# Optimization experiments

Measured on AMD Instinct MI355X. Metric: run time of the kernel, lower is better.

The kernel has to match this reference:

```python
import jax, jax.numpy as jnp
import numpy as np

N, E = 100000, 1600000
IN_CH, HID, HEADS, OUT_CH = 128, 32, 2, 40
NEG_SLOPE = 0.2
BN_EPS = 1e-5


def _param(key, shape, scale=0.1):
    return scale * jax.random.normal(key, shape, dtype=jnp.float32)


def setup_inputs() -> dict:
    key = jax.random.key(0)
    ks = jax.random.split(key, 24)
    x = jax.random.normal(ks[0], (N, IN_CH), dtype=jnp.float32)
    edge_index = jax.random.randint(ks[1], (2, E), 0, N, dtype=jnp.int32)
    d0 = HEADS * HID  # 64
    inp = {
        'x': x, 'edge_index': edge_index,
        # conv0: in 128 -> 32 per head, concat -> 64
        'W0': _param(ks[2], (IN_CH, HEADS * HID)),
        'as0': _param(ks[3], (HEADS, HID)), 'ad0': _param(ks[4], (HEADS, HID)),
        'b0': jnp.zeros((d0,), jnp.float32),
        'g0': jnp.ones((d0,), jnp.float32), 'bt0': jnp.zeros((d0,), jnp.float32),
        # conv1: 64 -> 32 per head, concat -> 64
        'W1': _param(ks[5], (d0, HEADS * HID)),
        'as1': _param(ks[6], (HEADS, HID)), 'ad1': _param(ks[7], (HEADS, HID)),
        'b1': jnp.zeros((d0,), jnp.float32),
        'g1': jnp.ones((d0,), jnp.float32), 'bt1': jnp.zeros((d0,), jnp.float32),
        # conv2: 64 -> 40 per head, mean over heads -> 40
        'W2': _param(ks[8], (d0, HEADS * OUT_CH)),
        'as2': _param(ks[9], (HEADS, OUT_CH)), 'ad2': _param(ks[10], (HEADS, OUT_CH)),
        'b2': jnp.zeros((OUT_CH,), jnp.float32),
    }
    return inp


def gat_conv(x, src, dst, W, a_src, a_dst, bias, out_ch, concat):
    n = x.shape[0]
    h = (x @ W).reshape(n, HEADS, out_ch)            # [N,H,C]
    alpha_src = jnp.sum(h * a_src, axis=-1)          # [N,H]
    alpha_dst = jnp.sum(h * a_dst, axis=-1)          # [N,H]
    e = jax.nn.leaky_relu(alpha_src[src] + alpha_dst[dst], NEG_SLOPE)  # [E,H]
    # softmax over incoming edges per destination node (self loops guarantee >=1 edge)
    m = jax.ops.segment_max(e, dst, num_segments=n)
    e = jnp.exp(e - m[dst])
    s = jax.ops.segment_sum(e, dst, num_segments=n)
    alpha = e / s[dst]                                # [E,H]
    msg = h[src] * alpha[:, :, None]                  # [E,H,C]
    out = jax.ops.segment_sum(msg, dst, num_segments=n)  # [N,H,C]
    out = out.reshape(n, HEADS * out_ch) if concat else out.mean(axis=1)
    return out + bias


def batch_norm(x, gamma, beta):
    mu = jnp.mean(x, axis=0)
    var = jnp.mean(jnp.square(x - mu), axis=0)
    return gamma * (x - mu) * jax.lax.rsqrt(var + BN_EPS) + beta


def reference(x, edge_index, W0, as0, ad0, b0, g0, bt0,
              W1, as1, ad1, b1, g1, bt1, W2, as2, ad2, b2):
    n = x.shape[0]
    loops = jnp.arange(n, dtype=edge_index.dtype)
    src = jnp.concatenate([edge_index[0], loops])
    dst = jnp.concatenate([edge_index[1], loops])
    h = gat_conv(x, src, dst, W0, as0, ad0, b0, HID, True)
    h = jax.nn.elu(batch_norm(h, g0, bt0))
    h = gat_conv(h, src, dst, W1, as1, ad1, b1, HID, True)
    h = jax.nn.elu(batch_norm(h, g1, bt1))
    return gat_conv(h, src, dst, W2, as2, ad2, b2, OUT_CH, False)
```

## Files before the change

### kernel.cpp

```cpp
#include <hip/hip_runtime.h>
#include <hip/hip_bf16.h>
#include <math.h>


#define NNODES 100000
#define NEDGES 1600000
#define ENTOT  (NEDGES + NNODES)
#define NEG_SLOPE 0.2f
#define BN_EPS 1e-5f

#define NRANGE 8
#define RSIZE  (NNODES/NRANGE)
#define BCAP   262144
#define PBLK   2048
#define NB2    32
#define BSL    8192

typedef unsigned short u16;
typedef unsigned int u32;
typedef unsigned long long u64;
typedef __attribute__((ext_vector_type(8))) short short8;
typedef __attribute__((ext_vector_type(4))) float f32x4;

__device__ __forceinline__ float b2f(u16 u){ union{u32 i; float f;} v; v.i=((u32)u)<<16; return v.f; }
__device__ __forceinline__ float blo(u32 u){ union{u32 i; float f;} v; v.i=u<<16; return v.f; }
__device__ __forceinline__ float bhi(u32 u){ union{u32 i; float f;} v; v.i=u&0xffff0000u; return v.f; }
__device__ __forceinline__ u16 f2b(float x){ __hip_bfloat16 b=__float2bfloat16(x); return *(u16*)&b; }
__device__ __forceinline__ float ldf(const void* p, int i, int f){
  return f ? ((const float*)p)[i] : b2f(((const u16*)p)[i]);
}

__global__ void k_detect(const u16* __restrict__ x, int* __restrict__ flag){
  __shared__ int bad;
  if(threadIdx.x==0) bad=0;
  __syncthreads();
  int cnt=0;
  for(int i=threadIdx.x;i<4096;i+=256){
    u16 v = x[2*i];
    int ex = (v>>7)&0xff;
    if(ex==0xff || (ex==0 && (v&0x7fff)!=0)) cnt++;
  }
  atomicAdd(&bad,cnt);
  __syncthreads();
  if(threadIdx.x==0) flag[0] = (bad>4)?1:0;
}

__global__ __launch_bounds__(256) void k_part2(
    const int* __restrict__ ei, int* __restrict__ gptr, u32* __restrict__ bkt){
  __shared__ int lcnt[NRANGE], gbase[NRANGE];
  int t=threadIdx.x;
  if(t<NRANGE) lcnt[t]=0;
  __syncthreads();
  const int CH=(ENTOT+PBLK-1)/PBLK;
  int beg=blockIdx.x*CH, end=beg+CH; if(end>ENTOT) end=ENTOT;
  int nd[4], ns[4], nr[4], ne=0;
  for(int i=beg+t; i<end; i+=256){
    int d=(i<NEDGES)? ei[NEDGES+i] : (i-NEDGES);
    int s=(i<NEDGES)? ei[i] : d;
    nd[ne]=d; ns[ne]=s; ne++;
  }
  #pragma unroll 4
  for(int k=0;k<ne;k++) nr[k]=atomicAdd(&lcnt[nd[k]/RSIZE],1);
  __syncthreads();
  if(t<NRANGE) gbase[t]=atomicAdd(&gptr[t],lcnt[t]);
  __syncthreads();
  #pragma unroll 4
  for(int k=0;k<ne;k++){
    int r=nd[k]/RSIZE;
    u32 e = ((u32)(nd[k]-r*RSIZE)<<17) | (u32)ns[k];
    __builtin_nontemporal_store(e, &bkt[(size_t)r*BCAP + gbase[r] + nr[k]]);
  }
}

__global__ __launch_bounds__(256) void k_hist4(
    const u32* __restrict__ bkt, const int* __restrict__ gptr, int* __restrict__ lhist){
  __shared__ int lh[RSIZE];
  int t=threadIdx.x;
  for(int i=t;i<RSIZE;i+=256) lh[i]=0;
  __syncthreads();
  int r = blockIdx.x & (NRANGE-1);
  int c = blockIdx.x >> 3;
  int n = gptr[r];
  int per=(n+NB2-1)/NB2;
  int beg=c*per, end=beg+per; if(end>n) end=n;
  const u32* bp = bkt + (size_t)r*BCAP;
  for(int i=beg+t;i<end;i+=256) atomicAdd(&lh[bp[i]>>17],1);
  __syncthreads();
  int* out = lhist + (size_t)(r*NB2+c)*RSIZE;
  for(int i=t;i<RSIZE;i+=256) out[i]=lh[i];
}

__global__ __launch_bounds__(256) void k_sumscan(int* __restrict__ lhist, int* __restrict__ cnt){
  int n = blockIdx.x*256 + threadIdx.x;
  if(n>=NNODES) return;
  int r = n/RSIZE, i = n - r*RSIZE;
  int* base = lhist + (size_t)r*NB2*RSIZE + i;
  int run=0;
  #pragma unroll 8
  for(int c=0;c<NB2;c++){
    int v = base[(size_t)c*RSIZE];
    base[(size_t)c*RSIZE] = run;
    run += v;
  }
  cnt[n]=run;
}

#define SCAN_M (NNODES+1)
#define SCAN_NB ((SCAN_M + 2047)/2048)

__global__ void k_scan_a(const int* __restrict__ cnt, int* __restrict__ bsum){
  __shared__ int red[256];
  int b=blockIdx.x, t=threadIdx.x;
  int base = b*2048 + t*8;
  int s=0;
  #pragma unroll
  for(int j=0;j<8;j++){ int idx=base+j; s += (idx<NNODES)? cnt[idx]:0; }
  red[t]=s; __syncthreads();
  for(int o=128;o>0;o>>=1){ if(t<o) red[t]+=red[t+o]; __syncthreads(); }
  if(t==0) bsum[b]=red[0];
}

__global__ void k_scan_b(int* bsum){
  if(threadIdx.x==0){
    int run=0;
    for(int i=0;i<SCAN_NB;i++){ int v=bsum[i]; bsum[i]=run; run+=v; }
  }
}

__global__ void k_scan_c(const int* __restrict__ cnt, const int* __restrict__ bsum,
                         int* __restrict__ row_ptr){
  __shared__ int lds[256];
  int b=blockIdx.x, t=threadIdx.x;
  int base=b*2048+t*8;
  int v[8]; int s=0;
  #pragma unroll
  for(int j=0;j<8;j++){ int idx=base+j; int x=(idx<NNODES)?cnt[idx]:0; v[j]=s; s+=x; }
  lds[t]=s; __syncthreads();
  for(int o=1;o<256;o<<=1){
    int other=0; if(t>=o) other=lds[t-o];
    __syncthreads();
    lds[t]+=other;
    __syncthreads();
  }
  int texcl = lds[t] - s;
  int off0 = bsum[b] + texcl;
  #pragma unroll
  for(int j=0;j<8;j++){ int idx=base+j; if(idx<SCAN_M) row_ptr[idx]=off0+v[j]; }
}

__global__ __launch_bounds__(256) void k_scatter4(
    const u32* __restrict__ bkt, const int* __restrict__ gptr,
    const int* __restrict__ row_ptr, const int* __restrict__ lhist,
    int* __restrict__ col){
  __shared__ int lofs[RSIZE];
  int t=threadIdx.x;
  int r = blockIdx.x & (NRANGE-1);
  int c = blockIdx.x >> 3;
  int lo = r*RSIZE;
  const int* cb = lhist + (size_t)(r*NB2+c)*RSIZE;
  for(int i=t;i<RSIZE;i+=256) lofs[i] = row_ptr[lo+i] + cb[i];
  __syncthreads();
  int n = gptr[r];
  int per=(n+NB2-1)/NB2;
  int beg=c*per, end=beg+per; if(end>n) end=n;
  const u32* bp = bkt + (size_t)r*BCAP;
  for(int i=beg+t;i<end;i+=256){
    u32 e=bp[i];
    int pos=atomicAdd(&lofs[e>>17],1);
    col[pos]=(int)(e & 0x1FFFF);
  }
}

__global__ __launch_bounds__(256) void k_binsort(
    const int* __restrict__ row_ptr, const int* __restrict__ col,
    int* __restrict__ col2){
  __shared__ int lcol[BSL];
  int t = threadIdx.x;
  int blk0 = blockIdx.x*256;
  int d1 = blk0+256; if(d1>NNODES) d1=NNODES;
  int s0 = row_ptr[blk0], s1 = row_ptr[d1];
  int n = s1 - s0;
  bool fit = (n<=BSL);
  if(fit){ for(int i=t;i<n;i+=256) lcol[i]=col[s0+i]; }
  __syncthreads();
  int d = blk0 + t;
  if(d<NNODES){
    int b0=row_ptr[d], b1=row_ptr[d+1];
    u64 cntp=0;
    for(int j=b0;j<b1;j++){
      int c = fit ? lcol[j-s0] : col[j];
      cntp += 1ull << ((c/RSIZE)*8);
    }
    u64 offp=0; u32 run=0;
    #pragma unroll
    for(int sb=0;sb<8;sb++){
      offp |= (u64)(run&0xffu) << (sb*8);
      run += (u32)((cntp >> (sb*8)) & 0xff);
    }
    for(int j=b0;j<b1;j++){
      int c = fit ? lcol[j-s0] : col[j];
      int sb = c/RSIZE;
      int pos = b0 + (int)((offp>>(sb*8))&0xff);
      offp += 1ull << (sb*8);
      col2[pos]=c;
    }
  }
}

template<int K, int OUTC, int HID, bool XEXT, bool BN>
__global__ __launch_bounds__(256) void k_gemm_mfma(
    const void* __restrict__ xin, const void* __restrict__ W,
    const void* __restrict__ avs, const void* __restrict__ avd,
    const float2* __restrict__ bnab,
    u16* __restrict__ hout, float* __restrict__ asrc, float* __restrict__ adst,
    const int* __restrict__ flagp)
{
  const int f = flagp[0];
  constexpr int KP = K+8;
  constexpr int RS = OUTC+8;
  constexpr int NT = OUTC/16;
  constexpr int KQ = K/32;
  __shared__ __align__(16) u16 WT[OUTC*KP];
  __shared__ __align__(16) u16 HROW[4*16*RS];
  __shared__ float AVb[2*OUTC];
  __shared__ float2 BB[K];
  int t=threadIdx.x;
  const u16* Wu=(const u16*)W; const float* Wf=(const float*)W;
  for(int i8=t*8; i8<K*OUTC; i8+=256*8){
    int k=i8/OUTC, c0=i8-k*OUTC;
    u16 w8[8];
    if(f){
      const float* wp=Wf+i8;
      float4 a=*(const float4*)wp, b=*(const float4*)(wp+4);
      w8[0]=f2b(a.x);w8[1]=f2b(a.y);w8[2]=f2b(a.z);w8[3]=f2b(a.w);
      w8[4]=f2b(b.x);w8[5]=f2b(b.y);w8[6]=f2b(b.z);w8[7]=f2b(b.w);
    } else {
      uint4 q=*(const uint4*)(Wu+i8);
      w8[0]=q.x&0xffff;w8[1]=q.x>>16;w8[2]=q.y&0xffff;w8[3]=q.y>>16;
      w8[4]=q.z&0xffff;w8[5]=q.z>>16;w8[6]=q.w&0xffff;w8[7]=q.w>>16;
    }
    #pragma unroll
    for(int u=0;u<8;u++) WT[(c0+u)*KP + k] = w8[u];
  }
  for(int idx=t; idx<2*OUTC; idx+=256)
    AVb[idx] = (idx<OUTC)? ldf(avs,idx,f) : ldf(avd,idx-OUTC,f);
  if(BN) for(int idx=t; idx<K; idx+=256) BB[idx]=bnab[idx];
  __syncthreads();

  int wv=t>>6, lane=t&63;
  int m=lane&15, quad=lane>>4;
  int grow0 = blockIdx.x*64 + wv*16;
  int growA = grow0 + m;
  bool avalid = growA < NNODES;
  int growC = avalid ? growA : 0;

  f32x4 acc[NT] = {};
  #pragma unroll
  for(int kq=0;kq<KQ;kq++){
    int k0 = kq*32 + quad*8;
    union{ u32 u[4]; short8 s8; } A;
    if(XEXT && f==1){
      const float* xr=(const float*)xin + (size_t)growC*K + k0;
      float4 p=*(const float4*)xr, q=*(const float4*)(xr+4);
      A.u[0]=f2b(p.x)|((u32)f2b(p.y)<<16);
      A.u[1]=f2b(p.z)|((u32)f2b(p.w)<<16);
      A.u[2]=f2b(q.x)|((u32)f2b(q.y)<<16);
      A.u[3]=f2b(q.z)|((u32)f2b(q.w)<<16);
    } else {
      uint4 q=*(const uint4*)((const u16*)xin + (size_t)growC*K + k0);
      A.u[0]=q.x; A.u[1]=q.y; A.u[2]=q.z; A.u[3]=q.w;
    }
    if(BN){
      #pragma unroll
      for(int j=0;j<4;j++){
        float lo=b2f(A.u[j]&0xffff), hi=b2f(A.u[j]>>16);
        float2 c1=BB[k0+2*j], c2=BB[k0+2*j+1];
        lo=c1.x*lo+c1.y; lo = lo>0.f? lo : __expf(lo)-1.f;
        hi=c2.x*hi+c2.y; hi = hi>0.f? hi : __expf(hi)-1.f;
        A.u[j]=f2b(lo)|((u32)f2b(hi)<<16);
      }
    }
    #pragma unroll
    for(int nt=0;nt<NT;nt++){
      union{ uint4 q; short8 s8; } Bf;
      Bf.q = *(const uint4*)&WT[(nt*16+m)*KP + k0];
      acc[nt] = __builtin_amdgcn_mfma_f32_16x16x32_bf16(A.s8, Bf.s8, acc[nt], 0,0,0);
    }
  }
  u16* hr = &HROW[wv*16*RS];
  #pragma unroll
  for(int nt=0;nt<NT;nt++){
    #pragma unroll
    for(int reg=0;reg<4;reg++)
      hr[(quad*4+reg)*RS + nt*16+m] = f2b(acc[nt][reg]);
  }
  __syncthreads();
  {
    int row=lane&15, task=quad, head=task&1, sd=task>>1;
    float p=0.f;
    const u16* hrow=&hr[row*RS + head*HID];
    const float* av=&AVb[sd*OUTC + head*HID];
    #pragma unroll 8
    for(int c=0;c<HID;c++) p += b2f(hrow[c])*av[c];
    int grow=grow0+row;
    if(grow<NNODES){ (sd? adst:asrc)[grow*2+head]=p; }
  }
  {
    constexpr int CH8 = OUTC/8;
    for(int idx=lane; idx<16*CH8; idx+=64){
      int rr=idx/CH8, c8=idx-rr*CH8;
      int grow=grow0+rr;
      if(grow<NNODES)
        *(uint4*)(hout + (size_t)grow*OUTC + c8*8) = *(const uint4*)&hr[rr*RS + c8*8];
    }
  }
}

template<int OUTC, bool FINAL>
__global__ __launch_bounds__(256) void k_aggf(
  const int* __restrict__ row_ptr, const int* __restrict__ col2,
  const u16* __restrict__ hin, const float* __restrict__ asrcf,
  const float2* __restrict__ adst2, const void* __restrict__ bias,
  u16* __restrict__ houtb, void* __restrict__ outv, const int* __restrict__ flagp)
{
  const int f = flagp[0];
  __shared__ float vbuf[FINAL?32:1][84];
  int t = threadIdx.x;
  int g  = t>>3;
  int cg = t&7;
  int rr = blockIdx.x & 7, jb = blockIdx.x >> 3;
  int lim = RSIZE - jb*32;
  bool ok = g < lim;
  int d = rr*RSIZE + jb*32 + g;
  int base=0, deg=0;
  float2 adv = make_float2(0.f,0.f);
  if(ok){
    base = row_ptr[d];
    deg  = row_ptr[d+1] - base;
    adv  = adst2[d];
  }
  const int* cp  = col2 + base;
  const u16* hcg = hin + cg*8;
  float acc[8]={0,0,0,0,0,0,0,0};

  if(!FINAL){
    int ho = (cg>=4)?1:0;
    float aown = ho ? adv.y : adv.x;
    float s=0.f;
    for(int ph=0; ph<4; ++ph){
      int beg = (deg*ph)>>2;
      int end = (deg*(ph+1))>>2;
      for(int j=beg; j<end; j+=2){
        int c0 = cp[j];
        bool v1 = (j+1)<end;
        int c1 = cp[v1 ? j+1 : j];
        float sa = asrcf[c0*2+ho];
        float sb = asrcf[c1*2+ho];
        uint4 h0 = *(const uint4*)(hcg + (size_t)c0*OUTC);
        uint4 h1 = *(const uint4*)(hcg + (size_t)c1*OUTC);
        float e0 = sa+aown; e0 = fmaxf(e0, NEG_SLOPE*e0); e0 = fminf(e0,60.f);
        float e1 = sb+aown; e1 = fmaxf(e1, NEG_SLOPE*e1); e1 = fminf(e1,60.f);
        float p0 = __expf(e0), p1 = __expf(e1);
        if(!v1) p1 = 0.f;
        s += p0 + p1;
        acc[0] += p0*blo(h0.x) + p1*blo(h1.x);
        acc[1] += p0*bhi(h0.x) + p1*bhi(h1.x);
        acc[2] += p0*blo(h0.y) + p1*blo(h1.y);
        acc[3] += p0*bhi(h0.y) + p1*bhi(h1.y);
        acc[4] += p0*blo(h0.z) + p1*blo(h1.z);
        acc[5] += p0*bhi(h0.z) + p1*bhi(h1.z);
        acc[6] += p0*blo(h0.w) + p1*blo(h1.w);
        acc[7] += p0*bhi(h0.w) + p1*bhi(h1.w);
      }
      __syncthreads();
    }
    float inv = s>0.f ? 1.f/s : 0.f;
    if(ok){
      u16 o8[8];
      #pragma unroll
      for(int k=0;k<8;k++) o8[k]=f2b(acc[k]*inv + ldf(bias,cg*8+k,f));
      uint4 ov;
      ov.x=(u32)o8[0]|((u32)o8[1]<<16); ov.y=(u32)o8[2]|((u32)o8[3]<<16);
      ov.z=(u32)o8[4]|((u32)o8[5]<<16); ov.w=(u32)o8[6]|((u32)o8[7]<<16);
      *(uint4*)(houtb + (size_t)d*64 + cg*8) = ov;
    }
  } else {
    const float2* asrc2 = (const float2*)asrcf;
    const u16* hxg = hin + 64 + cg*2;
    float accx0=0.f, accx1=0.f;
    float s0=0.f, s1=0.f;
    for(int ph=0; ph<4; ++ph){
      int beg = (deg*ph)>>2;
      int end = (deg*(ph+1))>>2;
      for(int j=beg; j<end; j+=2){
        int c0 = cp[j];
        bool v1 = (j+1)<end;
        int c1 = cp[v1 ? j+1 : j];
        float2 sa = asrc2[c0];
        float2 sv = asrc2[c1];
        const u16* hp0 = hcg + (size_t)c0*OUTC;
        const u16* hp1 = hcg + (size_t)c1*OUTC;
        uint4 h0 = *(const uint4*)hp0;
        uint4 h1 = *(const uint4*)hp1;
        float e0 = sa.x+adv.x; e0 = fmaxf(e0, NEG_SLOPE*e0); e0 = fminf(e0,60.f);
        float e1 = sa.y+adv.y; e1 = fmaxf(e1, NEG_SLOPE*e1); e1 = fminf(e1,60.f);
        float p0 = __expf(e0), p1 = __expf(e1);
        float q0 = sv.x+adv.x; q0 = fmaxf(q0, NEG_SLOPE*q0); q0 = fminf(q0,60.f);
        float q1 = sv.y+adv.y; q1 = fmaxf(q1, NEG_SLOPE*q1); q1 = fminf(q1,60.f);
        float r0 = __expf(q0), r1 = __expf(q1);
        if(!v1){ r0=0.f; r1=0.f; }
        s0 += p0 + r0; s1 += p1 + r1;
        float pa = (cg<5)? p0 : p1;
        float pb = (cg<5)? r0 : r1;
        acc[0] += pa*blo(h0.x) + pb*blo(h1.x);
        acc[1] += pa*bhi(h0.x) + pb*bhi(h1.x);
        acc[2] += pa*blo(h0.y) + pb*blo(h1.y);
        acc[3] += pa*bhi(h0.y) + pb*bhi(h1.y);
        acc[4] += pa*blo(h0.z) + pb*blo(h1.z);
        acc[5] += pa*bhi(h0.z) + pb*bhi(h1.z);
        acc[6] += pa*blo(h0.w) + pb*blo(h1.w);
        acc[7] += pa*bhi(h0.w) + pb*bhi(h1.w);
        ushort2 ha = *(const ushort2*)(hxg + (size_t)c0*OUTC);
        ushort2 hb = *(const ushort2*)(hxg + (size_t)c1*OUTC);
        accx0 += p1*b2f(ha.x) + r1*b2f(hb.x);
        accx1 += p1*b2f(ha.y) + r1*b2f(hb.y);
      }
      __syncthreads();
    }
    float inv0 = s0>0.f?1.f/s0:0.f, inv1 = s1>0.f?1.f/s1:0.f;
    if(ok){
      #pragma unroll
      for(int k=0;k<8;k++)
        vbuf[g][cg*8+k] = acc[k]*((cg<5)?inv0:inv1);
      vbuf[g][64+cg*2]   = accx0*inv1;
      vbuf[g][64+cg*2+1] = accx1*inv1;
    }
    __syncthreads();
    for(int idx=t; idx<32*40; idx+=256){
      int gg=idx/40, ch=idx-gg*40;
      if(gg<lim){
        int dd = rr*RSIZE + jb*32 + gg;
        float res = 0.5f*(vbuf[gg][ch] + vbuf[gg][40+ch]) + ldf(bias,ch,f);
        if(f) ((float*)outv)[(size_t)dd*40+ch] = res;
        else  ((__hip_bfloat16*)outv)[(size_t)dd*40+ch] = __float2bfloat16(res);
      }
    }
  }
}

__global__ __launch_bounds__(256) void k_bnstats(const u16* __restrict__ h, float* __restrict__ stats){
  __shared__ float red[4][128];
  int t=threadIdx.x; int c=t&63; int g=t>>6;
  float s=0.f,q=0.f;
  for(int r=blockIdx.x*4+g; r<NNODES; r+=gridDim.x*4){
    float v=b2f(h[(size_t)r*64+c]); s+=v; q+=v*v;
  }
  red[g][c]=s; red[g][64+c]=q;
  __syncthreads();
  if(t<128){
    float tot=red[0][t]+red[1][t]+red[2][t]+red[3][t];
    atomicAdd(&stats[t], tot);
  }
}

__global__ void k_bnfinal(const float* __restrict__ stats,
                          const void* __restrict__ gm, const void* __restrict__ bt,
                          float2* __restrict__ bnab, const int* __restrict__ flagp){
  const int f = flagp[0];
  int c=threadIdx.x;
  if(c>=64) return;
  float mu=stats[c]*(1.0f/NNODES);
  float var=stats[64+c]*(1.0f/NNODES)-mu*mu;
  var = var>0.f?var:0.f;
  float A = ldf(gm,c,f)*rsqrtf(var+BN_EPS);
  float B = ldf(bt,c,f) - A*mu;
  bnab[c]=make_float2(A,B);
}

extern "C" void kernel_launch(void* const* d_in, const int* in_sizes, int n_in,
                              void* d_out, int out_size, void* d_ws, size_t ws_size,
                              hipStream_t stream){
  const void* x  =d_in[0];
  const int* ei =(const int*)d_in[1];
  const void* W0 =d_in[2];  const void* as0=d_in[3];  const void* ad0=d_in[4];
  const void* b0 =d_in[5];  const void* g0 =d_in[6];  const void* bt0=d_in[7];
  const void* W1 =d_in[8];  const void* as1=d_in[9];  const void* ad1=d_in[10];
  const void* b1 =d_in[11]; const void* g1 =d_in[12]; const void* bt1=d_in[13];
  const void* W2 =d_in[14]; const void* as2=d_in[15]; const void* ad2=d_in[16];
  const void* b2 =d_in[17];

  char* ws=(char*)d_ws;
  size_t off=0;
  auto alloc=[&](size_t bytes)->void*{ void* p=ws+off; off+=(bytes+255)&~(size_t)255; return p; };
  int*    flag   =(int*)   alloc(256);
  int*    row_ptr=(int*)   alloc((size_t)(NNODES+1)*4);
  int*    cnt    =(int*)   alloc((size_t)NNODES*4);
  int*    colx   =(int*)   alloc((size_t)ENTOT*4);
  int*    colx2  =(int*)   alloc((size_t)ENTOT*4);
  int*    bsum   =(int*)   alloc((size_t)SCAN_NB*4);
  int*    gptr   =(int*)   alloc(256);
  u32*    bkt    =(u32*)   alloc((size_t)NRANGE*BCAP*4);
  u16*    hA     =(u16*)   alloc((size_t)100032*80*2);
  u16*    hB0    =(u16*)   alloc((size_t)100032*64*2);
  u16*    hB1    =(u16*)   alloc((size_t)100032*64*2);
  float*  asrc   =(float*) alloc((size_t)NNODES*2*4);
  float*  adst   =(float*) alloc((size_t)NNODES*2*4);
  float*  stats  =(float*) alloc(128*4);
  float2* bnab   =(float2*)alloc(64*8);
  int*    lhist  =(int*)hA;

  k_detect<<<1,256,0,stream>>>((const u16*)x, flag);

  (void)hipMemsetAsync(gptr,0,256,stream);
  k_part2  <<<PBLK,256,0,stream>>>(ei,gptr,bkt);
  k_hist4  <<<NRANGE*NB2,256,0,stream>>>(bkt,gptr,lhist);
  k_sumscan<<<(NNODES+255)/256,256,0,stream>>>(lhist,cnt);
  k_scan_a <<<SCAN_NB,256,0,stream>>>(cnt,bsum);
  k_scan_b <<<1,64,0,stream>>>(bsum);
  k_scan_c <<<SCAN_NB,256,0,stream>>>(cnt,bsum,row_ptr);
  k_scatter4<<<NRANGE*NB2,256,0,stream>>>(bkt,gptr,row_ptr,lhist,colx);
  k_binsort<<<(NNODES+255)/256,256,0,stream>>>(row_ptr,colx,colx2);

  int gG = (NNODES+63)/64;
  int gA = NRANGE * ((RSIZE + 31)/32);
  k_gemm_mfma<128,64,32,true ,false><<<gG,256,0,stream>>>(
      x,W0,as0,ad0,nullptr,hA,asrc,adst,flag);
  k_aggf<64,false><<<gA,256,0,stream>>>(row_ptr,colx2,hA,
      asrc,(const float2*)adst,b0,hB0,nullptr,flag);
  (void)hipMemsetAsync(stats,0,512,stream);
  k_bnstats<<<256,256,0,stream>>>(hB0,stats);
  k_bnfinal<<<1,64,0,stream>>>(stats,g0,bt0,bnab,flag);
  k_gemm_mfma<64,64,32,false,true ><<<gG,256,0,stream>>>(
      hB0,W1,as1,ad1,bnab,hA,asrc,adst,flag);
  k_aggf<64,false><<<gA,256,0,stream>>>(row_ptr,colx2,hA,
      asrc,(const float2*)adst,b1,hB1,nullptr,flag);
  (void)hipMemsetAsync(stats,0,512,stream);
  k_bnstats<<<256,256,0,stream>>>(hB1,stats);
  k_bnfinal<<<1,64,0,stream>>>(stats,g1,bt1,bnab,flag);
  k_gemm_mfma<64,80,40,false,true ><<<gG,256,0,stream>>>(
      hB1,W2,as2,ad2,bnab,hA,asrc,adst,flag);
  k_aggf<80,true ><<<gA,256,0,stream>>>(row_ptr,colx2,hA,
      asrc,(const float2*)adst,b2,nullptr,d_out,flag);

  (void)in_sizes;(void)n_in;(void)out_size;(void)ws_size;
}
```

Before: 466.1 us.

## Drop per-row source-range binsort and phased block-synchronized aggregation

Removes the k_binsort pass, which regrouped each node's neighbor list by source-node range, along with the four-phase loop with __syncthreads in the aggregation kernels that used that grouping to keep concurrent gathers within one source range. Aggregation now walks the unsorted CSR column list in a single loop. This saves one kernel launch, an extra column array and per-phase barriers, at the cost of losing the cache locality the phased, range-sorted gathers were designed to provide.

```diff
diff --git a/kernel.cpp b/kernel.cpp
--- a/kernel.cpp
+++ b/kernel.cpp
@@ -14,7 +14,6 @@
 #define BCAP   262144
 #define PBLK   2048
 #define NB2    32
-#define BSL    8192
 
 typedef unsigned short u16;
 typedef unsigned int u32;
@@ -168,42 +167,6 @@
     u32 e=bp[i];
     int pos=atomicAdd(&lofs[e>>17],1);
     col[pos]=(int)(e & 0x1FFFF);
-  }
-}
-
-__global__ __launch_bounds__(256) void k_binsort(
-    const int* __restrict__ row_ptr, const int* __restrict__ col,
-    int* __restrict__ col2){
-  __shared__ int lcol[BSL];
-  int t = threadIdx.x;
-  int blk0 = blockIdx.x*256;
-  int d1 = blk0+256; if(d1>NNODES) d1=NNODES;
-  int s0 = row_ptr[blk0], s1 = row_ptr[d1];
-  int n = s1 - s0;
-  bool fit = (n<=BSL);
-  if(fit){ for(int i=t;i<n;i+=256) lcol[i]=col[s0+i]; }
-  __syncthreads();
-  int d = blk0 + t;
-  if(d<NNODES){
-    int b0=row_ptr[d], b1=row_ptr[d+1];
-    u64 cntp=0;
-    for(int j=b0;j<b1;j++){
-      int c = fit ? lcol[j-s0] : col[j];
-      cntp += 1ull << ((c/RSIZE)*8);
-    }
-    u64 offp=0; u32 run=0;
-    #pragma unroll
-    for(int sb=0;sb<8;sb++){
-      offp |= (u64)(run&0xffu) << (sb*8);
-      run += (u32)((cntp >> (sb*8)) & 0xff);
-    }
-    for(int j=b0;j<b1;j++){
-      int c = fit ? lcol[j-s0] : col[j];
-      int sb = c/RSIZE;
-      int pos = b0 + (int)((offp>>(sb*8))&0xff);
-      offp += 1ull << (sb*8);
-      col2[pos]=c;
-    }
   }
 }
 
@@ -318,7 +281,7 @@
 
 template<int OUTC, bool FINAL>
 __global__ __launch_bounds__(256) void k_aggf(
-  const int* __restrict__ row_ptr, const int* __restrict__ col2,
+  const int* __restrict__ row_ptr, const int* __restrict__ col,
   const u16* __restrict__ hin, const float* __restrict__ asrcf,
   const float2* __restrict__ adst2, const void* __restrict__ bias,
   u16* __restrict__ houtb, void* __restrict__ outv, const int* __restrict__ flagp)
@@ -339,7 +302,7 @@
     deg  = row_ptr[d+1] - base;
     adv  = adst2[d];
   }
-  const int* cp  = col2 + base;
+  const int* cp  = col + base;
   const u16* hcg = hin + cg*8;
   float acc[8]={0,0,0,0,0,0,0,0};
 
@@ -347,32 +310,27 @@
     int ho = (cg>=4)?1:0;
     float aown = ho ? adv.y : adv.x;
     float s=0.f;
-    for(int ph=0; ph<4; ++ph){
-      int beg = (deg*ph)>>2;
-      int end = (deg*(ph+1))>>2;
-      for(int j=beg; j<end; j+=2){
-        int c0 = cp[j];
-        bool v1 = (j+1)<end;
-        int c1 = cp[v1 ? j+1 : j];
-        float sa = asrcf[c0*2+ho];
-        float sb = asrcf[c1*2+ho];
-        uint4 h0 = *(const uint4*)(hcg + (size_t)c0*OUTC);
-        uint4 h1 = *(const uint4*)(hcg + (size_t)c1*OUTC);
-        float e0 = sa+aown; e0 = fmaxf(e0, NEG_SLOPE*e0); e0 = fminf(e0,60.f);
-        float e1 = sb+aown; e1 = fmaxf(e1, NEG_SLOPE*e1); e1 = fminf(e1,60.f);
-        float p0 = __expf(e0), p1 = __expf(e1);
-        if(!v1) p1 = 0.f;
-        s += p0 + p1;
-        acc[0] += p0*blo(h0.x) + p1*blo(h1.x);
-        acc[1] += p0*bhi(h0.x) + p1*bhi(h1.x);
-        acc[2] += p0*blo(h0.y) + p1*blo(h1.y);
-        acc[3] += p0*bhi(h0.y) + p1*bhi(h1.y);
-        acc[4] += p0*blo(h0.z) + p1*blo(h1.z);
-        acc[5] += p0*bhi(h0.z) + p1*bhi(h1.z);
-        acc[6] += p0*blo(h0.w) + p1*blo(h1.w);
-        acc[7] += p0*bhi(h0.w) + p1*bhi(h1.w);
-      }
-      __syncthreads();
+    for(int j=0;j<deg;j+=2){
+      int c0 = cp[j];
+      bool v1 = (j+1)<deg;
+      int c1 = cp[v1 ? j+1 : j];
+      float sa = asrcf[c0*2+ho];
+      float sb = asrcf[c1*2+ho];
+      uint4 h0 = *(const uint4*)(hcg + (size_t)c0*OUTC);
+      uint4 h1 = *(const uint4*)(hcg + (size_t)c1*OUTC);
+      float e0 = sa+aown; e0 = fmaxf(e0, NEG_SLOPE*e0); e0 = fminf(e0,60.f);
+      float e1 = sb+aown; e1 = fmaxf(e1, NEG_SLOPE*e1); e1 = fminf(e1,60.f);
+      float p0 = __expf(e0), p1 = __expf(e1);
+      if(!v1) p1 = 0.f;
+      s += p0 + p1;
+      acc[0] += p0*blo(h0.x) + p1*blo(h1.x);
+      acc[1] += p0*bhi(h0.x) + p1*bhi(h1.x);
+      acc[2] += p0*blo(h0.y) + p1*blo(h1.y);
+      acc[3] += p0*bhi(h0.y) + p1*bhi(h1.y);
+      acc[4] += p0*blo(h0.z) + p1*blo(h1.z);
+      acc[5] += p0*bhi(h0.z) + p1*bhi(h1.z);
+      acc[6] += p0*blo(h0.w) + p1*blo(h1.w);
+      acc[7] += p0*bhi(h0.w) + p1*bhi(h1.w);
     }
     float inv = s>0.f ? 1.f/s : 0.f;
     if(ok){
@@ -389,43 +347,38 @@
     const u16* hxg = hin + 64 + cg*2;
     float accx0=0.f, accx1=0.f;
     float s0=0.f, s1=0.f;
-    for(int ph=0; ph<4; ++ph){
-      int beg = (deg*ph)>>2;
-      int end = (deg*(ph+1))>>2;
-      for(int j=beg; j<end; j+=2){
-        int c0 = cp[j];
-        bool v1 = (j+1)<end;
-        int c1 = cp[v1 ? j+1 : j];
-        float2 sa = asrc2[c0];
-        float2 sv = asrc2[c1];
-        const u16* hp0 = hcg + (size_t)c0*OUTC;
-        const u16* hp1 = hcg + (size_t)c1*OUTC;
-        uint4 h0 = *(const uint4*)hp0;
-        uint4 h1 = *(const uint4*)hp1;
-        float e0 = sa.x+adv.x; e0 = fmaxf(e0, NEG_SLOPE*e0); e0 = fminf(e0,60.f);
-        float e1 = sa.y+adv.y; e1 = fmaxf(e1, NEG_SLOPE*e1); e1 = fminf(e1,60.f);
-        float p0 = __expf(e0), p1 = __expf(e1);
-        float q0 = sv.x+adv.x; q0 = fmaxf(q0, NEG_SLOPE*q0); q0 = fminf(q0,60.f);
-        float q1 = sv.y+adv.y; q1 = fmaxf(q1, NEG_SLOPE*q1); q1 = fminf(q1,60.f);
-        float r0 = __expf(q0), r1 = __expf(q1);
-        if(!v1){ r0=0.f; r1=0.f; }
-        s0 += p0 + r0; s1 += p1 + r1;
-        float pa = (cg<5)? p0 : p1;
-        float pb = (cg<5)? r0 : r1;
-        acc[0] += pa*blo(h0.x) + pb*blo(h1.x);
-        acc[1] += pa*bhi(h0.x) + pb*bhi(h1.x);
-        acc[2] += pa*blo(h0.y) + pb*blo(h1.y);
-        acc[3] += pa*bhi(h0.y) + pb*bhi(h1.y);
-        acc[4] += pa*blo(h0.z) + pb*blo(h1.z);
-        acc[5] += pa*bhi(h0.z) + pb*bhi(h1.z);
-        acc[6] += pa*blo(h0.w) + pb*blo(h1.w);
-        acc[7] += pa*bhi(h0.w) + pb*bhi(h1.w);
-        ushort2 ha = *(const ushort2*)(hxg + (size_t)c0*OUTC);
-        ushort2 hb = *(const ushort2*)(hxg + (size_t)c1*OUTC);
-        accx0 += p1*b2f(ha.x) + r1*b2f(hb.x);
-        accx1 += p1*b2f(ha.y) + r1*b2f(hb.y);
-      }
-      __syncthreads();
+    for(int j=0;j<deg;j+=2){
+      int c0 = cp[j];
+      bool v1 = (j+1)<deg;
+      int c1 = cp[v1 ? j+1 : j];
+      float2 sa = asrc2[c0];
+      float2 sv = asrc2[c1];
+      const u16* hp0 = hcg + (size_t)c0*OUTC;
+      const u16* hp1 = hcg + (size_t)c1*OUTC;
+      uint4 h0 = *(const uint4*)hp0;
+      uint4 h1 = *(const uint4*)hp1;
+      float e0 = sa.x+adv.x; e0 = fmaxf(e0, NEG_SLOPE*e0); e0 = fminf(e0,60.f);
+      float e1 = sa.y+adv.y; e1 = fmaxf(e1, NEG_SLOPE*e1); e1 = fminf(e1,60.f);
+      float p0 = __expf(e0), p1 = __expf(e1);
+      float q0 = sv.x+adv.x; q0 = fmaxf(q0, NEG_SLOPE*q0); q0 = fminf(q0,60.f);
+      float q1 = sv.y+adv.y; q1 = fmaxf(q1, NEG_SLOPE*q1); q1 = fminf(q1,60.f);
+      float r0 = __expf(q0), r1 = __expf(q1);
+      if(!v1){ r0=0.f; r1=0.f; }
+      s0 += p0 + r0; s1 += p1 + r1;
+      float pa = (cg<5)? p0 : p1;
+      float pb = (cg<5)? r0 : r1;
+      acc[0] += pa*blo(h0.x) + pb*blo(h1.x);
+      acc[1] += pa*bhi(h0.x) + pb*bhi(h1.x);
+      acc[2] += pa*blo(h0.y) + pb*blo(h1.y);
+      acc[3] += pa*bhi(h0.y) + pb*bhi(h1.y);
+      acc[4] += pa*blo(h0.z) + pb*blo(h1.z);
+      acc[5] += pa*bhi(h0.z) + pb*bhi(h1.z);
+      acc[6] += pa*blo(h0.w) + pb*blo(h1.w);
+      acc[7] += pa*bhi(h0.w) + pb*bhi(h1.w);
+      ushort2 ha = *(const ushort2*)(hxg + (size_t)c0*OUTC);
+      ushort2 hb = *(const ushort2*)(hxg + (size_t)c1*OUTC);
+      accx0 += p1*b2f(ha.x) + r1*b2f(hb.x);
+      accx1 += p1*b2f(ha.y) + r1*b2f(hb.y);
     }
     float inv0 = s0>0.f?1.f/s0:0.f, inv1 = s1>0.f?1.f/s1:0.f;
     if(ok){
@@ -496,7 +449,6 @@
   int*    row_ptr=(int*)   alloc((size_t)(NNODES+1)*4);
   int*    cnt    =(int*)   alloc((size_t)NNODES*4);
   int*    colx   =(int*)   alloc((size_t)ENTOT*4);
-  int*    colx2  =(int*)   alloc((size_t)ENTOT*4);
   int*    bsum   =(int*)   alloc((size_t)SCAN_NB*4);
   int*    gptr   =(int*)   alloc(256);
   u32*    bkt    =(u32*)   alloc((size_t)NRANGE*BCAP*4);
@@ -519,27 +471,26 @@
   k_scan_b <<<1,64,0,stream>>>(bsum);
   k_scan_c <<<SCAN_NB,256,0,stream>>>(cnt,bsum,row_ptr);
   k_scatter4<<<NRANGE*NB2,256,0,stream>>>(bkt,gptr,row_ptr,lhist,colx);
-  k_binsort<<<(NNODES+255)/256,256,0,stream>>>(row_ptr,colx,colx2);
 
   int gG = (NNODES+63)/64;
   int gA = NRANGE * ((RSIZE + 31)/32);
   k_gemm_mfma<128,64,32,true ,false><<<gG,256,0,stream>>>(
       x,W0,as0,ad0,nullptr,hA,asrc,adst,flag);
-  k_aggf<64,false><<<gA,256,0,stream>>>(row_ptr,colx2,hA,
+  k_aggf<64,false><<<gA,256,0,stream>>>(row_ptr,colx,hA,
       asrc,(const float2*)adst,b0,hB0,nullptr,flag);
   (void)hipMemsetAsync(stats,0,512,stream);
   k_bnstats<<<256,256,0,stream>>>(hB0,stats);
   k_bnfinal<<<1,64,0,stream>>>(stats,g0,bt0,bnab,flag);
   k_gemm_mfma<64,64,32,false,true ><<<gG,256,0,stream>>>(
       hB0,W1,as1,ad1,bnab,hA,asrc,adst,flag);
-  k_aggf<64,false><<<gA,256,0,stream>>>(row_ptr,colx2,hA,
+  k_aggf<64,false><<<gA,256,0,stream>>>(row_ptr,colx,hA,
       asrc,(const float2*)adst,b1,hB1,nullptr,flag);
   (void)hipMemsetAsync(stats,0,512,stream);
   k_bnstats<<<256,256,0,stream>>>(hB1,stats);
   k_bnfinal<<<1,64,0,stream>>>(stats,g1,bt1,bnab,flag);
   k_gemm_mfma<64,80,40,false,true ><<<gG,256,0,stream>>>(
       hB1,W2,as2,ad2,bnab,hA,asrc,adst,flag);
-  k_aggf<80,true ><<<gA,256,0,stream>>>(row_ptr,colx2,hA,
+  k_aggf<80,true ><<<gA,256,0,stream>>>(row_ptr,colx,hA,
       asrc,(const float2*)adst,b2,nullptr,d_out,flag);
 
   (void)in_sizes;(void)n_in;(void)out_size;(void)ws_size;
```

Measured after the change: 447.1 us. -4.1%, faster.
